# Optimization experiments

Measured on AMD Instinct MI355X. Metric: run time of the kernel, lower is better.

## Reference

```python
import jax, jax.numpy as jnp
import numpy as np

HEAD_DIM = 64
N_HEADS = 32
LRPE_BASE = 512


def _rotate_half(x):
    x1, x2 = jnp.split(x, 2, axis=-1)
    return jnp.concatenate((-x2, x1), axis=-1)


def _cos_sin(L, dtype):
    inv_freq = 1.0 / (LRPE_BASE ** (jnp.arange(0, HEAD_DIM, 2, dtype=jnp.float32) / HEAD_DIM))
    t = jnp.arange(L, dtype=jnp.float32)
    freqs = t[:, None] * inv_freq[None, :]          # (L, hd/2)
    emb = jnp.concatenate((freqs, freqs), axis=-1)  # (L, hd)
    return jnp.cos(emb).astype(dtype), jnp.sin(emb).astype(dtype)


def setup_inputs() -> dict:
    key = jax.random.key(0)
    k1, k2, k3 = jax.random.split(key, 3)
    B, L, D = 2, 2048, 2048
    x = jax.random.normal(k1, (B, L, D), dtype=jnp.float32)
    wqkv = jax.random.normal(k2, (3 * D, D), dtype=jnp.float32) * (D ** -0.5)
    wo = jax.random.normal(k3, (D, D), dtype=jnp.float32) * (D ** -0.5)
    return {"x": x, "wqkv": wqkv, "wo": wo}


def reference(x, wqkv, wo):
    B, L, D = x.shape
    H, hd = N_HEADS, HEAD_DIM
    qkv = x @ wqkv.T                                   # (B, L, 3D)
    qkv = qkv.reshape(B, L, 3, H, hd)
    q, k, v = qkv[:, :, 0], qkv[:, :, 1], qkv[:, :, 2]  # (B, L, H, hd)

    cos, sin = _cos_sin(L, x.dtype)                    # (L, hd)
    cos = cos[None, :, None, :]
    sin = sin[None, :, None, :]
    q = q * cos + _rotate_half(q) * sin
    k = k * cos + _rotate_half(k) * sin

    scale = hd ** -0.5
    scores = jnp.einsum("bqhd,bkhd->bhqk", q, k) * scale  # (B, H, L, L)
    causal = jnp.triu(jnp.ones((L, L), dtype=bool), k=1)
    scores = jnp.where(causal[None, None], -jnp.inf, scores)
    attn = jax.nn.softmax(scores, axis=-1)
    out = jnp.einsum("bhqk,bkhd->bqhd", attn, v)       # (B, L, H, hd)
    out = out.reshape(B, L, D)
    return out @ wo.T
```

## Files before the change

kernel.cpp:

```cpp
#include <hip/hip_runtime.h>

using u16 = unsigned short;
using u32 = unsigned int;

typedef __attribute__((ext_vector_type(8))) __bf16 bf16x8;
typedef __attribute__((ext_vector_type(4))) __bf16 bf16x4;
typedef __attribute__((ext_vector_type(4))) float f32x4;

__device__ __forceinline__ u16 f2bf(float f) {
  u32 u = __builtin_bit_cast(u32, f);
  u = (u + 0x7fffu + ((u >> 16) & 1u)) >> 16;
  return (u16)u;
}
__device__ __forceinline__ float bf2f(u16 h) {
  u32 u = ((u32)h) << 16;
  return __builtin_bit_cast(float, u);
}

__device__ __forceinline__ float exp2_fast(float x) {
  float r; asm("v_exp_f32 %0, %1" : "=v"(r) : "v"(x)); return r;
}

#define GLDS16(gp, lp)                                                              \
  __builtin_amdgcn_global_load_lds((const __attribute__((address_space(1))) void*)(gp), \
                                   (__attribute__((address_space(3))) void*)(lp), 16, 0, 0)

__global__ void cvt_kernel(const float* __restrict__ in, u16* __restrict__ out, int n4) {
  int idx = blockIdx.x * blockDim.x + threadIdx.x;
  int stride = gridDim.x * blockDim.x;
  for (int i = idx; i < n4; i += stride) {
    float4 f = ((const float4*)in)[i];
    ushort4 o;
    o.x = f2bf(f.x); o.y = f2bf(f.y); o.z = f2bf(f.z); o.w = f2bf(f.w);
    ((ushort4*)out)[i] = o;
  }
}

template <int OUT_BF16>
__global__ __launch_bounds__(512, 2) void gemm256(const u16* __restrict__ A,
                                                  const u16* __restrict__ B,
                                                  void* __restrict__ Cv,
                                                  int M, int N, int K) {
  extern __shared__ u16 lds[];
  const int tid = threadIdx.x;
  const int w = tid >> 6, lane = tid & 63;
  const int g = lane >> 4, lo = lane & 15;
  const int wm = (w >> 2) * 128, wn = (w & 3) * 64;
  const int nwg = gridDim.x * gridDim.y;
  const int lid = blockIdx.y * gridDim.x + blockIdx.x;
  const int cpx = nwg >> 3;
  const int swz = (lid & 7) * cpx + (lid >> 3);
  const int bxs = swz % gridDim.x, bys = swz / gridDim.x;
  const int bm = bys * 256, bn = bxs * 256;
  const int NT = K >> 6;

  auto stage_half = [&](int mat, int buf, int half, int kt) {
    if (kt >= NT) return;
    const u16* src = mat ? B : A;
    const int rbase = (mat ? bn : bm) + half * 128;
    u16* lbase0 = lds + mat * 32768 + buf * 16384 + half * 8192;
#pragma unroll
    for (int j = 0; j < 2; ++j) {
      const int f = j * 512 + tid;
      const int rl = f >> 3, cl = f & 7;
      const int cg = cl ^ (rl & 7);
      const u16* gp = src + (size_t)(rbase + rl) * K + kt * 64 + cg * 8;
      GLDS16(gp, lbase0 + (j * 512 + w * 64) * 8);
    }
  };
  auto lda = [&](int buf, int q, int m2, int ks) -> bf16x8 {
    const int row = wm + q * 32 + m2 * 16 + lo;
    const int cl = (ks * 4 + g) ^ (row & 7);
    return *(const bf16x8*)(lds + buf * 16384 + row * 64 + cl * 8);
  };
  auto ldb = [&](int buf, int n, int ks) -> bf16x8 {
    const int row = wn + n * 16 + lo;
    const int cl = (ks * 4 + g) ^ (row & 7);
    return *(const bf16x8*)(lds + 32768 + buf * 16384 + row * 64 + cl * 8);
  };

  f32x4 acc[8][4] = {};
  bf16x8 bfrag[4][2];

#define PHASE(buf, q, LDB, smat, sbuf, shalf, stile, vm)                                    \
  do {                                                                                      \
    bf16x8 af[2][2];                                                                        \
    _Pragma("unroll") for (int m2_ = 0; m2_ < 2; ++m2_)                                     \
    _Pragma("unroll") for (int ks_ = 0; ks_ < 2; ++ks_)                                     \
      af[m2_][ks_] = lda(buf, q, m2_, ks_);                                                 \
    if (LDB) {                                                                              \
      _Pragma("unroll") for (int n_ = 0; n_ < 4; ++n_)                                      \
      _Pragma("unroll") for (int ks_ = 0; ks_ < 2; ++ks_)                                   \
        bfrag[n_][ks_] = ldb(buf, n_, ks_);                                                 \
    }                                                                                       \
    stage_half(smat, sbuf, shalf, stile);                                                   \
    if ((vm) == 4) asm volatile("s_waitcnt vmcnt(4)");                                      \
    else if ((vm) == 0) asm volatile("s_waitcnt vmcnt(0)");                                 \
    __builtin_amdgcn_s_barrier();                                                           \
    asm volatile("s_waitcnt lgkmcnt(0)");                                                   \
    __builtin_amdgcn_sched_barrier(0);                                                      \
    __builtin_amdgcn_s_setprio(1);                                                          \
    _Pragma("unroll") for (int m2_ = 0; m2_ < 2; ++m2_)                                     \
    _Pragma("unroll") for (int n_ = 0; n_ < 4; ++n_)                                        \
    _Pragma("unroll") for (int ks_ = 0; ks_ < 2; ++ks_)                                     \
      acc[(q) * 2 + m2_][n_] = __builtin_amdgcn_mfma_f32_16x16x32_bf16(                     \
          af[m2_][ks_], bfrag[n_][ks_], acc[(q) * 2 + m2_][n_], 0, 0, 0);                   \
    __builtin_amdgcn_s_setprio(0);                                                          \
    __builtin_amdgcn_sched_barrier(0);                                                      \
    __builtin_amdgcn_s_barrier();                                                           \
  } while (0)

  stage_half(1, 0, 0, 0); stage_half(1, 0, 1, 0);
  stage_half(0, 0, 0, 0); stage_half(0, 0, 1, 0);
  stage_half(1, 1, 0, 1); stage_half(1, 1, 1, 1);
  asm volatile("s_waitcnt vmcnt(4)");
  __builtin_amdgcn_s_barrier();

  const int NITER = NT >> 1;
  for (int i = 0; i < NITER - 1; ++i) {
    const int to = 2 * i + 1, te = 2 * i + 2, tn = 2 * i + 3;
    PHASE(0, 0, 1, 0, 1, 0, to, -1);
    PHASE(0, 1, 0, 0, 1, 1, to, -1);
    PHASE(0, 2, 0, 1, 0, 0, te, -1);
    PHASE(0, 3, 0, 1, 0, 1, te, 4);
    PHASE(1, 0, 1, 0, 0, 0, te, -1);
    PHASE(1, 1, 0, 0, 0, 1, te, -1);
    PHASE(1, 2, 0, 1, 1, 0, tn, -1);
    PHASE(1, 3, 0, 1, 1, 1, tn, 4);
  }
  {
    const int to = NT - 1;
    PHASE(0, 0, 1, 0, 1, 0, to, -1);
    PHASE(0, 1, 0, 0, 1, 1, to, -1);
    PHASE(0, 2, 0, 1, 0, 0, NT, -1);
    PHASE(0, 3, 0, 1, 0, 1, NT, 0);
    PHASE(1, 0, 1, 0, 0, 0, NT, -1);
    PHASE(1, 1, 0, 0, 0, 1, NT, -1);
    PHASE(1, 2, 0, 1, 1, 0, NT, -1);
    PHASE(1, 3, 0, 1, 1, 1, NT, -1);
  }
#undef PHASE

#pragma unroll
  for (int m = 0; m < 8; ++m)
#pragma unroll
    for (int r = 0; r < 4; ++r) {
      const int row = bm + wm + m * 16 + g * 4 + r;
#pragma unroll
      for (int n = 0; n < 4; ++n) {
        const int col = bn + wn + n * 16 + lo;
        float v = acc[m][n][r];
        if (OUT_BF16) ((u16*)Cv)[(size_t)row * N + col] = f2bf(v);
        else ((float*)Cv)[(size_t)row * N + col] = v;
      }
    }
}

__global__ __launch_bounds__(256) void rope_kernel(const u16* __restrict__ qkv,
                                                   u16* __restrict__ Q,
                                                   u16* __restrict__ Ko,
                                                   u16* __restrict__ VT) {
  const int bh = blockIdx.x;
  const int lt = blockIdx.y;
  const int b = bh >> 5, h = bh & 31;
  const int tid = threadIdx.x;
  const int l0 = lt * 64;
  const float QSC = 0.18033688011f;

  const int i = tid & 31;
  const float invf = exp2f(-(float)i * 0.28125f);
#pragma unroll
  for (int it = 0; it < 8; ++it) {
    const int l = (tid >> 5) + it * 8;
    const int m = b * 2048 + l0 + l;
    float s, c;
    __sincosf((float)(l0 + l) * invf, &s, &c);
    const int base = m * 6144 + h * 64 + i;
    float qlo = bf2f(qkv[base]), qhi = bf2f(qkv[base + 32]);
    float klo = bf2f(qkv[base + 2048]), khi = bf2f(qkv[base + 2048 + 32]);
    const int ob = (bh * 2048 + l0 + l) * 64 + i;
    Q[ob] = f2bf((qlo * c - qhi * s) * QSC);
    Q[ob + 32] = f2bf((qhi * c + qlo * s) * QSC);
    Ko[ob] = f2bf(klo * c - khi * s);
    Ko[ob + 32] = f2bf(khi * c + klo * s);
  }

  __shared__ alignas(16) u16 vs[64][72];
#pragma unroll
  for (int it = 0; it < 2; ++it) {
    const int c = tid * 2 + it;
    const int l = c >> 3, off = (c & 7) * 8;
    const int m = b * 2048 + l0 + l;
    *(uint4*)&vs[l][off] = *(const uint4*)&qkv[m * 6144 + 4096 + h * 64 + off];
  }
  __syncthreads();
#pragma unroll
  for (int it = 0; it < 2; ++it) {
    const int c = tid * 2 + it;
    const int d = c >> 3, lc = (c & 7) * 8;
    u32 w0 = (u32)vs[lc + 0][d] | ((u32)vs[lc + 1][d] << 16);
    u32 w1 = (u32)vs[lc + 2][d] | ((u32)vs[lc + 3][d] << 16);
    u32 w2 = (u32)vs[lc + 4][d] | ((u32)vs[lc + 5][d] << 16);
    u32 w3 = (u32)vs[lc + 6][d] | ((u32)vs[lc + 7][d] << 16);
    uint4 pk; pk.x = w0; pk.y = w1; pk.z = w2; pk.w = w3;
    *(uint4*)&VT[(size_t)(bh * 64 + d) * 2048 + l0 + lc] = pk;
  }
}

__global__ __launch_bounds__(256) void flash_kernel(const u16* __restrict__ Q,
                                                    const u16* __restrict__ K,
                                                    const u16* __restrict__ V,
                                                    u16* __restrict__ O) {
  __shared__ alignas(16) u16 KVs[2][2][64][64];
  __shared__ alignas(16) u16 Ps2[4][2][2][64][8];
  const int bid = blockIdx.x;
  const int xcd = bid & 7, slot = bid >> 3;
  const int bh = xcd * 8 + (slot & 7);
  const int pair = slot >> 3;
  const int b = bh >> 5, h = bh & 31;
  const int tid = threadIdx.x;
  const int w = tid >> 6, lane = tid & 63;
  const int g = lane >> 4, lo = lane & 15;
  const size_t bh2048 = (size_t)bh * 2048;
  const int srow = tid >> 3;
  const int sc8 = tid & 7;

  auto stage = [&](int buf, int kv0) {
#pragma unroll
    for (int p = 0; p < 2; ++p) {
      const int r = p * 32 + srow;
      const int col8 = sc8 ^ (r & 7);
      const u16* gk = K + (bh2048 + kv0 + r) * 64 + col8 * 8;
      const u16* gv = V + ((size_t)bh * 64 + r) * 2048 + kv0 + col8 * 8;
      u16* lbase = &KVs[buf][0][0][0] + p * 2048 + w * 512;
      GLDS16(gk, lbase);
      GLDS16(gv, lbase + 4096);
    }
  };

  for (int seg = 0; seg < 2; ++seg) {
    const int qt = seg ? 15 - pair : pair;
    const int qbase = qt * 128 + w * 32;
    const int ntile = 2 * qt + 2;

    bf16x8 qf[2][2];
#pragma unroll
    for (int qj = 0; qj < 2; ++qj)
#pragma unroll
      for (int ks = 0; ks < 2; ++ks)
        qf[qj][ks] = *(const bf16x8*)(Q + (bh2048 + qbase + qj * 16 + lo) * 64 + ks * 32 + g * 8);

    float mo[2] = {-1e30f, -1e30f};
    float ls[2] = {0.f, 0.f};
    f32x4 oacc[2][4] = {};

    stage(0, 0);
    __syncthreads();

    for (int t = 0; t < ntile; ++t) {
      const int cur = t & 1;
      const int kv0 = t * 64;
      if (t + 1 < ntile) stage(cur ^ 1, kv0 + 64);

      f32x4 st[4][2] = {};
#pragma unroll
      for (int kvi = 0; kvi < 4; ++kvi)
#pragma unroll
        for (int ks = 0; ks < 2; ++ks) {
          bf16x8 kf = *(const bf16x8*)&KVs[cur][0][kvi * 16 + lo][(ks * 32 + g * 8) ^ ((lo & 7) << 3)];
#pragma unroll
          for (int qj = 0; qj < 2; ++qj)
            st[kvi][qj] = __builtin_amdgcn_mfma_f32_16x16x32_bf16(kf, qf[qj][ks], st[kvi][qj], 0, 0, 0);
        }

      float corr2[2];
#pragma unroll
      for (int qj = 0; qj < 2; ++qj) {
        const int q = qbase + qj * 16 + lo;
        float tmax = -1e30f;
#pragma unroll
        for (int kvi = 0; kvi < 4; ++kvi)
#pragma unroll
          for (int r = 0; r < 4; ++r) {
            const int kv = kv0 + kvi * 16 + g * 4 + r;
            float s = st[kvi][qj][r];
            s = (kv <= q) ? s : -1e30f;
            st[kvi][qj][r] = s;
            tmax = fmaxf(tmax, s);
          }
        tmax = fmaxf(tmax, __shfl_xor(tmax, 16));
        tmax = fmaxf(tmax, __shfl_xor(tmax, 32));
        const float mn = fmaxf(mo[qj], tmax);
        const float corr = exp2_fast(mo[qj] - mn);
        mo[qj] = mn;
        float psum = 0.f;
#pragma unroll
        for (int kvi = 0; kvi < 4; ++kvi) {
          float p0 = exp2_fast(st[kvi][qj][0] - mn);
          float p1 = exp2_fast(st[kvi][qj][1] - mn);
          float p2 = exp2_fast(st[kvi][qj][2] - mn);
          float p3 = exp2_fast(st[kvi][qj][3] - mn);
          psum += (p0 + p1) + (p2 + p3);
          bf16x4 pk;
          pk[0] = (__bf16)p0; pk[1] = (__bf16)p1; pk[2] = (__bf16)p2; pk[3] = (__bf16)p3;
          *(bf16x4*)&Ps2[w][qj][kvi >> 1][((kvi & 1) * 2 + (g >> 1)) * 16 + lo][(g & 1) * 4] = pk;
        }
        psum += __shfl_xor(psum, 16);
        psum += __shfl_xor(psum, 32);
        ls[qj] = ls[qj] * corr + psum;
        corr2[qj] = corr;
      }

#pragma unroll
      for (int qi = 0; qi < 2; ++qi)
#pragma unroll
        for (int r = 0; r < 4; ++r) {
          const float cc = __shfl(corr2[qi], g * 4 + r);
#pragma unroll
          for (int ni = 0; ni < 4; ++ni) oacc[qi][ni][r] *= cc;
        }

      asm volatile("" ::: "memory");

      bf16x8 pa[2][2];
#pragma unroll
      for (int qi = 0; qi < 2; ++qi)
#pragma unroll
        for (int ks = 0; ks < 2; ++ks)
          pa[qi][ks] = *(const bf16x8*)&Ps2[w][qi][ks][lane][0];
#pragma unroll
      for (int ks = 0; ks < 2; ++ks)
#pragma unroll
        for (int ni = 0; ni < 4; ++ni) {
          bf16x8 vb = *(const bf16x8*)&KVs[cur][1][ni * 16 + lo][(ks * 32 + g * 8) ^ ((lo & 7) << 3)];
#pragma unroll
          for (int qi = 0; qi < 2; ++qi)
            oacc[qi][ni] = __builtin_amdgcn_mfma_f32_16x16x32_bf16(pa[qi][ks], vb, oacc[qi][ni], 0, 0, 0);
        }
      __syncthreads();
    }

#pragma unroll
    for (int qi = 0; qi < 2; ++qi) {
      const float linv = 1.0f / ls[qi];
#pragma unroll
      for (int r = 0; r < 4; ++r) {
        const float li = __shfl(linv, g * 4 + r);
        const int q = qbase + qi * 16 + g * 4 + r;
        const size_t rowoff = (size_t)(b * 2048 + q) * 2048 + h * 64;
#pragma unroll
        for (int ni = 0; ni < 4; ++ni)
          O[rowoff + ni * 16 + lo] = f2bf(oacc[qi][ni][r] * li);
      }
    }
  }
}

extern "C" void kernel_launch(void* const* d_in, const int* in_sizes, int n_in,
                              void* d_out, int out_size, void* d_ws, size_t ws_size,
                              hipStream_t stream) {
  const float* x = (const float*)d_in[0];
  const float* wqkv = (const float*)d_in[1];
  const float* wo = (const float*)d_in[2];
  float* out = (float*)d_out;

  u16* xb = (u16*)d_ws;
  u16* wqkvb = xb + (size_t)8388608;
  u16* wob = wqkvb + (size_t)12582912;
  u16* qkv = wob + (size_t)4194304;
  u16* qr = qkv + (size_t)25165824;
  u16* kr = qr + (size_t)8388608;
  u16* vt = kr + (size_t)8388608;
  u16* aout = xb;

  hipFuncSetAttribute((const void*)gemm256<1>, hipFuncAttributeMaxDynamicSharedMemorySize, 131072);
  hipFuncSetAttribute((const void*)gemm256<0>, hipFuncAttributeMaxDynamicSharedMemorySize, 131072);

  cvt_kernel<<<1024, 256, 0, stream>>>(x, xb, 8388608 / 4);
  cvt_kernel<<<1024, 256, 0, stream>>>(wqkv, wqkvb, 12582912 / 4);
  cvt_kernel<<<512, 256, 0, stream>>>(wo, wob, 4194304 / 4);

  gemm256<1><<<dim3(24, 16), 512, 131072, stream>>>(xb, wqkvb, qkv, 4096, 6144, 2048);

  rope_kernel<<<dim3(64, 32), 256, 0, stream>>>(qkv, qr, kr, vt);

  flash_kernel<<<dim3(512), 256, 0, stream>>>(qr, kr, vt, aout);

  gemm256<0><<<dim3(8, 16), 512, 131072, stream>>>(aout, wob, out, 4096, 2048, 2048);
}
```

Measured before the change: 403.7 us.

## Narrow output GEMM tile, skip causal mask off-diagonal, lazy softmax rescale

```diff
diff --git a/kernel.cpp b/kernel.cpp
--- a/kernel.cpp
+++ b/kernel.cpp
@@ -36,7 +36,7 @@
   }
 }
 
-template <int OUT_BF16>
+template <int OUT_BF16, int NB>
 __global__ __launch_bounds__(512, 2) void gemm256(const u16* __restrict__ A,
                                                   const u16* __restrict__ B,
                                                   void* __restrict__ Cv,
@@ -45,22 +45,24 @@
   const int tid = threadIdx.x;
   const int w = tid >> 6, lane = tid & 63;
   const int g = lane >> 4, lo = lane & 15;
-  const int wm = (w >> 2) * 128, wn = (w & 3) * 64;
+  const int wm = (w >> 2) * 128, wn = (w & 3) * (NB * 16);
   const int nwg = gridDim.x * gridDim.y;
   const int lid = blockIdx.y * gridDim.x + blockIdx.x;
   const int cpx = nwg >> 3;
   const int swz = (lid & 7) * cpx + (lid >> 3);
   const int bxs = swz % gridDim.x, bys = swz / gridDim.x;
-  const int bm = bys * 256, bn = bxs * 256;
+  const int bm = bys * 256, bn = bxs * (NB * 64);
   const int NT = K >> 6;
 
   auto stage_half = [&](int mat, int buf, int half, int kt) {
     if (kt >= NT) return;
+    const int rows_half = mat ? NB * 32 : 128;
+    const int nloads = rows_half >> 6;
     const u16* src = mat ? B : A;
-    const int rbase = (mat ? bn : bm) + half * 128;
-    u16* lbase0 = lds + mat * 32768 + buf * 16384 + half * 8192;
-#pragma unroll
-    for (int j = 0; j < 2; ++j) {
+    const int rbase = (mat ? bn : bm) + half * rows_half;
+    u16* lbase0 = lds + (mat ? 32768 + buf * (NB * 4096) : buf * 16384) + half * rows_half * 64;
+#pragma unroll
+    for (int j = 0; j < nloads; ++j) {
       const int f = j * 512 + tid;
       const int rl = f >> 3, cl = f & 7;
       const int cg = cl ^ (rl & 7);
@@ -76,11 +78,11 @@
   auto ldb = [&](int buf, int n, int ks) -> bf16x8 {
     const int row = wn + n * 16 + lo;
     const int cl = (ks * 4 + g) ^ (row & 7);
-    return *(const bf16x8*)(lds + 32768 + buf * 16384 + row * 64 + cl * 8);
+    return *(const bf16x8*)(lds + 32768 + buf * (NB * 4096) + row * 64 + cl * 8);
   };
 
-  f32x4 acc[8][4] = {};
-  bf16x8 bfrag[4][2];
+  f32x4 acc[8][NB] = {};
+  bf16x8 bfrag[NB][2];
 
 #define PHASE(buf, q, LDB, smat, sbuf, shalf, stile, vm)                                    \
   do {                                                                                      \
@@ -89,19 +91,21 @@
     _Pragma("unroll") for (int ks_ = 0; ks_ < 2; ++ks_)                                     \
       af[m2_][ks_] = lda(buf, q, m2_, ks_);                                                 \
     if (LDB) {                                                                              \
-      _Pragma("unroll") for (int n_ = 0; n_ < 4; ++n_)                                      \
+      _Pragma("unroll") for (int n_ = 0; n_ < NB; ++n_)                                     \
       _Pragma("unroll") for (int ks_ = 0; ks_ < 2; ++ks_)                                   \
         bfrag[n_][ks_] = ldb(buf, n_, ks_);                                                 \
     }                                                                                       \
     stage_half(smat, sbuf, shalf, stile);                                                   \
-    if ((vm) == 4) asm volatile("s_waitcnt vmcnt(4)");                                      \
-    else if ((vm) == 0) asm volatile("s_waitcnt vmcnt(0)");                                 \
+    if ((vm) == 0) asm volatile("s_waitcnt vmcnt(0)");                                      \
+    else if ((vm) == 2) asm volatile("s_waitcnt vmcnt(2)");                                 \
+    else if ((vm) == 4) asm volatile("s_waitcnt vmcnt(4)");                                 \
+    if (LDB) asm volatile("s_waitcnt lgkmcnt(8)");                                          \
     __builtin_amdgcn_s_barrier();                                                           \
     asm volatile("s_waitcnt lgkmcnt(0)");                                                   \
     __builtin_amdgcn_sched_barrier(0);                                                      \
     __builtin_amdgcn_s_setprio(1);                                                          \
     _Pragma("unroll") for (int m2_ = 0; m2_ < 2; ++m2_)                                     \
-    _Pragma("unroll") for (int n_ = 0; n_ < 4; ++n_)                                        \
+    _Pragma("unroll") for (int n_ = 0; n_ < NB; ++n_)                                       \
     _Pragma("unroll") for (int ks_ = 0; ks_ < 2; ++ks_)                                     \
       acc[(q) * 2 + m2_][n_] = __builtin_amdgcn_mfma_f32_16x16x32_bf16(                     \
           af[m2_][ks_], bfrag[n_][ks_], acc[(q) * 2 + m2_][n_], 0, 0, 0);                   \
@@ -113,7 +117,8 @@
   stage_half(1, 0, 0, 0); stage_half(1, 0, 1, 0);
   stage_half(0, 0, 0, 0); stage_half(0, 0, 1, 0);
   stage_half(1, 1, 0, 1); stage_half(1, 1, 1, 1);
-  asm volatile("s_waitcnt vmcnt(4)");
+  if (NB == 4) asm volatile("s_waitcnt vmcnt(4)");
+  else asm volatile("s_waitcnt vmcnt(2)");
   __builtin_amdgcn_s_barrier();
 
   const int NITER = NT >> 1;
@@ -122,11 +127,11 @@
     PHASE(0, 0, 1, 0, 1, 0, to, -1);
     PHASE(0, 1, 0, 0, 1, 1, to, -1);
     PHASE(0, 2, 0, 1, 0, 0, te, -1);
-    PHASE(0, 3, 0, 1, 0, 1, te, 4);
+    PHASE(0, 3, 0, 1, 0, 1, te, NB);
     PHASE(1, 0, 1, 0, 0, 0, te, -1);
     PHASE(1, 1, 0, 0, 0, 1, te, -1);
     PHASE(1, 2, 0, 1, 1, 0, tn, -1);
-    PHASE(1, 3, 0, 1, 1, 1, tn, 4);
+    PHASE(1, 3, 0, 1, 1, 1, tn, NB);
   }
   {
     const int to = NT - 1;
@@ -147,7 +152,7 @@
     for (int r = 0; r < 4; ++r) {
       const int row = bm + wm + m * 16 + g * 4 + r;
 #pragma unroll
-      for (int n = 0; n < 4; ++n) {
+      for (int n = 0; n < NB; ++n) {
         const int col = bn + wn + n * 16 + lo;
         float v = acc[m][n][r];
         if (OUT_BF16) ((u16*)Cv)[(size_t)row * N + col] = f2bf(v);
@@ -242,6 +247,7 @@
     const int qt = seg ? 15 - pair : pair;
     const int qbase = qt * 128 + w * 32;
     const int ntile = 2 * qt + 2;
+    const int nfree = 2 * qt;
 
     bf16x8 qf[2][2];
 #pragma unroll
@@ -273,26 +279,43 @@
             st[kvi][qj] = __builtin_amdgcn_mfma_f32_16x16x32_bf16(kf, qf[qj][ks], st[kvi][qj], 0, 0, 0);
         }
 
+      const bool need_mask = (t >= nfree);
       float corr2[2];
+      int skipall = 1;
 #pragma unroll
       for (int qj = 0; qj < 2; ++qj) {
         const int q = qbase + qj * 16 + lo;
         float tmax = -1e30f;
-#pragma unroll
-        for (int kvi = 0; kvi < 4; ++kvi)
-#pragma unroll
-          for (int r = 0; r < 4; ++r) {
-            const int kv = kv0 + kvi * 16 + g * 4 + r;
-            float s = st[kvi][qj][r];
-            s = (kv <= q) ? s : -1e30f;
-            st[kvi][qj][r] = s;
-            tmax = fmaxf(tmax, s);
-          }
+        if (need_mask) {
+#pragma unroll
+          for (int kvi = 0; kvi < 4; ++kvi)
+#pragma unroll
+            for (int r = 0; r < 4; ++r) {
+              const int kv = kv0 + kvi * 16 + g * 4 + r;
+              float s = st[kvi][qj][r];
+              s = (kv <= q) ? s : -1e30f;
+              st[kvi][qj][r] = s;
+              tmax = fmaxf(tmax, s);
+            }
+        } else {
+#pragma unroll
+          for (int kvi = 0; kvi < 4; ++kvi)
+#pragma unroll
+            for (int r = 0; r < 4; ++r) tmax = fmaxf(tmax, st[kvi][qj][r]);
+        }
         tmax = fmaxf(tmax, __shfl_xor(tmax, 16));
         tmax = fmaxf(tmax, __shfl_xor(tmax, 32));
-        const float mn = fmaxf(mo[qj], tmax);
-        const float corr = exp2_fast(mo[qj] - mn);
-        mo[qj] = mn;
+        const int sk = __all((int)(tmax <= mo[qj] + 11.54f));
+        float mn;
+        if (sk) {
+          mn = mo[qj];
+          corr2[qj] = 1.0f;
+        } else {
+          mn = fmaxf(mo[qj], tmax);
+          corr2[qj] = exp2_fast(mo[qj] - mn);
+          mo[qj] = mn;
+          skipall = 0;
+        }
         float psum = 0.f;
 #pragma unroll
         for (int kvi = 0; kvi < 4; ++kvi) {
@@ -307,18 +330,19 @@
         }
         psum += __shfl_xor(psum, 16);
         psum += __shfl_xor(psum, 32);
-        ls[qj] = ls[qj] * corr + psum;
-        corr2[qj] = corr;
+        ls[qj] = ls[qj] * corr2[qj] + psum;
       }
 
-#pragma unroll
-      for (int qi = 0; qi < 2; ++qi)
-#pragma unroll
-        for (int r = 0; r < 4; ++r) {
-          const float cc = __shfl(corr2[qi], g * 4 + r);
-#pragma unroll
-          for (int ni = 0; ni < 4; ++ni) oacc[qi][ni][r] *= cc;
-        }
+      if (!skipall) {
+#pragma unroll
+        for (int qi = 0; qi < 2; ++qi)
+#pragma unroll
+          for (int r = 0; r < 4; ++r) {
+            const float cc = __shfl(corr2[qi], g * 4 + r);
+#pragma unroll
+            for (int ni = 0; ni < 4; ++ni) oacc[qi][ni][r] *= cc;
+          }
+      }
 
       asm volatile("" ::: "memory");
 
@@ -373,18 +397,18 @@
   u16* vt = kr + (size_t)8388608;
   u16* aout = xb;
 
-  hipFuncSetAttribute((const void*)gemm256<1>, hipFuncAttributeMaxDynamicSharedMemorySize, 131072);
-  hipFuncSetAttribute((const void*)gemm256<0>, hipFuncAttributeMaxDynamicSharedMemorySize, 131072);
+  hipFuncSetAttribute((const void*)gemm256<1, 4>, hipFuncAttributeMaxDynamicSharedMemorySize, 131072);
+  hipFuncSetAttribute((const void*)gemm256<0, 2>, hipFuncAttributeMaxDynamicSharedMemorySize, 98304);
 
   cvt_kernel<<<1024, 256, 0, stream>>>(x, xb, 8388608 / 4);
   cvt_kernel<<<1024, 256, 0, stream>>>(wqkv, wqkvb, 12582912 / 4);
   cvt_kernel<<<512, 256, 0, stream>>>(wo, wob, 4194304 / 4);
 
-  gemm256<1><<<dim3(24, 16), 512, 131072, stream>>>(xb, wqkvb, qkv, 4096, 6144, 2048);
+  gemm256<1, 4><<<dim3(24, 16), 512, 131072, stream>>>(xb, wqkvb, qkv, 4096, 6144, 2048);
 
   rope_kernel<<<dim3(64, 32), 256, 0, stream>>>(qkv, qr, kr, vt);
 
   flash_kernel<<<dim3(512), 256, 0, stream>>>(qr, kr, vt, aout);
 
-  gemm256<0><<<dim3(8, 16), 512, 131072, stream>>>(aout, wob, out, 4096, 2048, 2048);
-}
+  gemm256<0, 2><<<dim3(16, 16), 512, 98304, stream>>>(aout, wob, out, 4096, 2048, 2048);
+}
```

New measurement: 381.0 us. -5.6%, faster.
